# Optimization experiments

Measured on AMD Instinct MI355X. Metric: run time of the kernel, lower is better.

## Reference

```python
import jax, jax.numpy as jnp
from jax import lax
import numpy as np

HIDDEN = 2
INPUT = 1
NUM_CLASSES = 1
SEQ = 4
BATCH = 2097152


def setup_inputs() -> dict:
    key = jax.random.key(0)
    ks = jax.random.split(key, 7)
    s_ih = 1.0 / np.sqrt(HIDDEN)
    inp = {
        "x": jax.random.normal(ks[0], (BATCH, SEQ, INPUT), dtype=jnp.float32),
        # PyTorch nn.LSTM params: gate order [i, f, g, o], init U(-1/sqrt(H), 1/sqrt(H))
        "W_ih": jax.random.uniform(ks[1], (4 * HIDDEN, INPUT), jnp.float32, -s_ih, s_ih),
        "W_hh": jax.random.uniform(ks[2], (4 * HIDDEN, HIDDEN), jnp.float32, -s_ih, s_ih),
        "b_ih": jax.random.uniform(ks[3], (4 * HIDDEN,), jnp.float32, -s_ih, s_ih),
        "b_hh": jax.random.uniform(ks[4], (4 * HIDDEN,), jnp.float32, -s_ih, s_ih),
        "W_fc": jax.random.uniform(ks[5], (NUM_CLASSES, HIDDEN), jnp.float32, -s_ih, s_ih),
        "b_fc": jax.random.uniform(ks[6], (NUM_CLASSES,), jnp.float32, -s_ih, s_ih),
    }
    return inp


def _lstm_fc(x, W_ih, W_hh, b_ih, b_hh, W_fc, b_fc):
    B = x.shape[0]
    H = W_hh.shape[1]
    xt = jnp.swapaxes(x, 0, 1)  # [T, B, I]
    # Precompute input contribution to all 4 gates for every step: [T, B, 4H]
    xg = jnp.einsum('tbi,gi->tbg', xt, W_ih) + (b_ih + b_hh)

    def step(carry, xg_t):
        h, c = carry
        gates = xg_t + h @ W_hh.T  # [B, 4H]
        i, f, g, o = jnp.split(gates, 4, axis=-1)
        i = jax.nn.sigmoid(i)
        f = jax.nn.sigmoid(f)
        g = jnp.tanh(g)
        o = jax.nn.sigmoid(o)
        c = f * c + i * g
        h = o * jnp.tanh(c)
        return (h, c), None

    h0 = jnp.zeros((B, H), dtype=x.dtype)
    c0 = jnp.zeros((B, H), dtype=x.dtype)
    (h_T, _), _ = lax.scan(step, (h0, c0), xg)
    # fc applied to the final hidden state h_out (num_layers=1)
    return h_T @ W_fc.T + b_fc  # [B, num_classes]


def reference(x, W_ih, W_hh, b_ih, b_hh, W_fc, b_fc):
    return _lstm_fc(x, W_ih, W_hh, b_ih, b_hh, W_fc, b_fc)
```

## Files before the change

### kernel.cpp

```cpp
#include <hip/hip_runtime.h>
#include <hip/hip_bf16.h>

#define TABN 4352

__device__ __forceinline__ float gclamp(float y) {
    return __builtin_amdgcn_fmed3f(y, 0.0f, 4351.0f);
}

__global__ __launch_bounds__(256) void lstm_fc_nn(
    const float4* __restrict__ x4,
    const float*  __restrict__ W_ih,
    const float*  __restrict__ W_hh,
    const float*  __restrict__ b_ih,
    const float*  __restrict__ b_hh,
    const float*  __restrict__ W_fc,
    const float*  __restrict__ b_fc,
    float* __restrict__ out,
    int B)
{
    __shared__ float tab[TABN];
    for (int i = threadIdx.x; i < TABN; i += 256) {
        const float xv = fmaf((float)i, 0.00390625f, -8.0f);
        tab[i] = __fdividef(1.0f, 1.0f + __expf(-xv));
    }
    __syncthreads();

    float ws[8], w0[8], w1[8], bb[8];
#pragma unroll
    for (int g = 0; g < 8; ++g) {
        const float s = (g == 4 || g == 5) ? 512.0f : 256.0f;
        ws[g] = s * W_ih[g];
        w0[g] = s * W_hh[2 * g];
        w1[g] = s * W_hh[2 * g + 1];
        bb[g] = fmaf(s, b_ih[g] + b_hh[g], 2048.5f);
    }
    const float wfc0 = W_fc[0], wfc1 = W_fc[1], bfc = b_fc[0];

    const int half = B >> 1;
    const int tid = blockIdx.x * blockDim.x + threadIdx.x;
    if (tid >= half) return;

    const float4 xa = x4[tid];
    const float4 xb = x4[tid + half];
    const float xs[2][4] = {{xa.x, xa.y, xa.z, xa.w}, {xb.x, xb.y, xb.z, xb.w}};

    float h0[2], h1[2], d0[2], d1[2];

#pragma unroll
    for (int e = 0; e < 2; ++e) {
        const float yi0 = fmaf(ws[0], xs[e][0], bb[0]);
        const float yi1 = fmaf(ws[1], xs[e][0], bb[1]);
        const float yg0 = fmaf(ws[4], xs[e][0], bb[4]);
        const float yg1 = fmaf(ws[5], xs[e][0], bb[5]);
        const float yo0 = fmaf(ws[6], xs[e][0], bb[6]);
        const float yo1 = fmaf(ws[7], xs[e][0], bb[7]);
        const float si0 = tab[(unsigned)yi0];
        const float si1 = tab[(unsigned)yi1];
        const float sg0 = tab[(unsigned)gclamp(yg0)];
        const float sg1 = tab[(unsigned)gclamp(yg1)];
        const float so0 = tab[(unsigned)yo0];
        const float so1 = tab[(unsigned)yo1];
        d0[e] = si0 * fmaf(4.0f, sg0, -2.0f);
        d1[e] = si1 * fmaf(4.0f, sg1, -2.0f);
        const float sd0 = tab[(unsigned)fmaf(d0[e], 256.0f, 2048.5f)];
        const float sd1 = tab[(unsigned)fmaf(d1[e], 256.0f, 2048.5f)];
        h0[e] = fmaf(2.0f, so0 * sd0, -so0);
        h1[e] = fmaf(2.0f, so1 * sd1, -so1);
    }

#pragma unroll
    for (int t = 1; t < 4; ++t) {
#pragma unroll
        for (int e = 0; e < 2; ++e) {
            float y[8];
#pragma unroll
            for (int g = 0; g < 8; ++g)
                y[g] = fmaf(ws[g], xs[e][t],
                       fmaf(w0[g], h0[e],
                       fmaf(w1[g], h1[e], bb[g])));
            const float si0 = tab[(unsigned)y[0]];
            const float si1 = tab[(unsigned)y[1]];
            const float sf0 = tab[(unsigned)y[2]];
            const float sf1 = tab[(unsigned)y[3]];
            const float sg0 = tab[(unsigned)gclamp(y[4])];
            const float sg1 = tab[(unsigned)gclamp(y[5])];
            const float so0 = tab[(unsigned)y[6]];
            const float so1 = tab[(unsigned)y[7]];
            d0[e] = fmaf(sf0, d0[e], si0 * fmaf(4.0f, sg0, -2.0f));
            d1[e] = fmaf(sf1, d1[e], si1 * fmaf(4.0f, sg1, -2.0f));
            const float sd0 = tab[(unsigned)fmaf(d0[e], 256.0f, 2048.5f)];
            const float sd1 = tab[(unsigned)fmaf(d1[e], 256.0f, 2048.5f)];
            h0[e] = fmaf(2.0f, so0 * sd0, -so0);
            h1[e] = fmaf(2.0f, so1 * sd1, -so1);
        }
    }

    out[tid]        = fmaf(wfc0, h0[0], fmaf(wfc1, h1[0], bfc));
    out[tid + half] = fmaf(wfc0, h0[1], fmaf(wfc1, h1[1], bfc));
}

extern "C" void kernel_launch(void* const* d_in, const int* in_sizes, int n_in,
                              void* d_out, int out_size, void* d_ws, size_t ws_size,
                              hipStream_t stream) {
    const float4* x4   = (const float4*)d_in[0];
    const float*  W_ih = (const float*)d_in[1];
    const float*  W_hh = (const float*)d_in[2];
    const float*  b_ih = (const float*)d_in[3];
    const float*  b_hh = (const float*)d_in[4];
    const float*  W_fc = (const float*)d_in[5];
    const float*  b_fc = (const float*)d_in[6];
    float* out = (float*)d_out;

    const int B = out_size;
    const int half = B >> 1;
    const int block = 256;
    const int grid = (half + block - 1) / block;
    lstm_fc_nn<<<grid, block, 0, stream>>>(x4, W_ih, W_hh, b_ih, b_hh,
                                           W_fc, b_fc, out, B);
}
```

Baseline: 25.00 us.

## Replace sigmoid LUT with replicated bank-conflict-free linearly interpolated table

Swaps the 4352-entry nearest-neighbour sigmoid table for a 256-entry table that stores each value with its slope and interpolates linearly. Each entry is replicated 16 times, and each thread reads the copy chosen by its lane index, so lanes in a wave fall on different LDS banks and bank conflicts on the data-dependent lookups drop. The input scales and biases are rescaled to match the coarser table. In exchange, each lookup costs extra ALU work (fraction and fma) and moves 8 bytes instead of 4, LDS use rises to about 32KB per block, and the interpolated values differ in accuracy from before.

```diff
diff --git a/kernel.cpp b/kernel.cpp
--- a/kernel.cpp
+++ b/kernel.cpp
@@ -1,13 +1,20 @@
 #include <hip/hip_runtime.h>
 #include <hip/hip_bf16.h>
 
-#define TABN 4352
+
+__device__ __forceinline__ float lutl(const float2* __restrict__ tab2,
+                                      unsigned copy, float y) {
+    const unsigned iy = (unsigned)y;
+    const float    fy = y - (float)iy;
+    const float2   vs = tab2[iy * 16u + copy];
+    return fmaf(vs.y, fy, vs.x);
+}
 
 __device__ __forceinline__ float gclamp(float y) {
-    return __builtin_amdgcn_fmed3f(y, 0.0f, 4351.0f);
+    return __builtin_amdgcn_fmed3f(y, 0.0f, 255.999f);
 }
 
-__global__ __launch_bounds__(256) void lstm_fc_nn(
+__global__ __launch_bounds__(256) void lstm_fc_cfree(
     const float4* __restrict__ x4,
     const float*  __restrict__ W_ih,
     const float*  __restrict__ W_hh,
@@ -18,24 +25,37 @@
     float* __restrict__ out,
     int B)
 {
-    __shared__ float tab[TABN];
-    for (int i = threadIdx.x; i < TABN; i += 256) {
-        const float xv = fmaf((float)i, 0.00390625f, -8.0f);
-        tab[i] = __fdividef(1.0f, 1.0f + __expf(-xv));
+    __shared__ float2 tab2[256 * 16];
+    __shared__ float  vtmp[257];
+
+    {
+        const int t = threadIdx.x;
+        const float xv = fmaf((float)t, 0.0625f, -8.0f);
+        vtmp[t] = __fdividef(1.0f, 1.0f + __expf(-xv));
+        if (t == 0) vtmp[256] = __fdividef(1.0f, 1.0f + __expf(-8.0f));
+        __syncthreads();
+        const float val = vtmp[t];
+        const float slp = vtmp[t + 1] - val;
+#pragma unroll
+        for (int j = 0; j < 16; ++j) {
+            const int c = (t + j) & 15;
+            tab2[t * 16 + c] = make_float2(val, slp);
+        }
+        __syncthreads();
     }
-    __syncthreads();
 
     float ws[8], w0[8], w1[8], bb[8];
 #pragma unroll
     for (int g = 0; g < 8; ++g) {
-        const float s = (g == 4 || g == 5) ? 512.0f : 256.0f;
+        const float s = (g == 4 || g == 5) ? 32.0f : 16.0f;
         ws[g] = s * W_ih[g];
         w0[g] = s * W_hh[2 * g];
         w1[g] = s * W_hh[2 * g + 1];
-        bb[g] = fmaf(s, b_ih[g] + b_hh[g], 2048.5f);
+        bb[g] = fmaf(s, b_ih[g] + b_hh[g], 128.0f);
     }
     const float wfc0 = W_fc[0], wfc1 = W_fc[1], bfc = b_fc[0];
 
+    const unsigned copy = threadIdx.x & 15u;
     const int half = B >> 1;
     const int tid = blockIdx.x * blockDim.x + threadIdx.x;
     if (tid >= half) return;
@@ -50,20 +70,20 @@
     for (int e = 0; e < 2; ++e) {
         const float yi0 = fmaf(ws[0], xs[e][0], bb[0]);
         const float yi1 = fmaf(ws[1], xs[e][0], bb[1]);
-        const float yg0 = fmaf(ws[4], xs[e][0], bb[4]);
-        const float yg1 = fmaf(ws[5], xs[e][0], bb[5]);
+        const float yg0 = gclamp(fmaf(ws[4], xs[e][0], bb[4]));
+        const float yg1 = gclamp(fmaf(ws[5], xs[e][0], bb[5]));
         const float yo0 = fmaf(ws[6], xs[e][0], bb[6]);
         const float yo1 = fmaf(ws[7], xs[e][0], bb[7]);
-        const float si0 = tab[(unsigned)yi0];
-        const float si1 = tab[(unsigned)yi1];
-        const float sg0 = tab[(unsigned)gclamp(yg0)];
-        const float sg1 = tab[(unsigned)gclamp(yg1)];
-        const float so0 = tab[(unsigned)yo0];
-        const float so1 = tab[(unsigned)yo1];
+        const float si0 = lutl(tab2, copy, yi0);
+        const float si1 = lutl(tab2, copy, yi1);
+        const float sg0 = lutl(tab2, copy, yg0);
+        const float sg1 = lutl(tab2, copy, yg1);
+        const float so0 = lutl(tab2, copy, yo0);
+        const float so1 = lutl(tab2, copy, yo1);
         d0[e] = si0 * fmaf(4.0f, sg0, -2.0f);
         d1[e] = si1 * fmaf(4.0f, sg1, -2.0f);
-        const float sd0 = tab[(unsigned)fmaf(d0[e], 256.0f, 2048.5f)];
-        const float sd1 = tab[(unsigned)fmaf(d1[e], 256.0f, 2048.5f)];
+        const float sd0 = lutl(tab2, copy, fmaf(d0[e], 16.0f, 128.0f));
+        const float sd1 = lutl(tab2, copy, fmaf(d1[e], 16.0f, 128.0f));
         h0[e] = fmaf(2.0f, so0 * sd0, -so0);
         h1[e] = fmaf(2.0f, so1 * sd1, -so1);
     }
@@ -78,18 +98,18 @@
                 y[g] = fmaf(ws[g], xs[e][t],
                        fmaf(w0[g], h0[e],
                        fmaf(w1[g], h1[e], bb[g])));
-            const float si0 = tab[(unsigned)y[0]];
-            const float si1 = tab[(unsigned)y[1]];
-            const float sf0 = tab[(unsigned)y[2]];
-            const float sf1 = tab[(unsigned)y[3]];
-            const float sg0 = tab[(unsigned)gclamp(y[4])];
-            const float sg1 = tab[(unsigned)gclamp(y[5])];
-            const float so0 = tab[(unsigned)y[6]];
-            const float so1 = tab[(unsigned)y[7]];
+            const float si0 = lutl(tab2, copy, y[0]);
+            const float si1 = lutl(tab2, copy, y[1]);
+            const float sf0 = lutl(tab2, copy, y[2]);
+            const float sf1 = lutl(tab2, copy, y[3]);
+            const float sg0 = lutl(tab2, copy, gclamp(y[4]));
+            const float sg1 = lutl(tab2, copy, gclamp(y[5]));
+            const float so0 = lutl(tab2, copy, y[6]);
+            const float so1 = lutl(tab2, copy, y[7]);
             d0[e] = fmaf(sf0, d0[e], si0 * fmaf(4.0f, sg0, -2.0f));
             d1[e] = fmaf(sf1, d1[e], si1 * fmaf(4.0f, sg1, -2.0f));
-            const float sd0 = tab[(unsigned)fmaf(d0[e], 256.0f, 2048.5f)];
-            const float sd1 = tab[(unsigned)fmaf(d1[e], 256.0f, 2048.5f)];
+            const float sd0 = lutl(tab2, copy, fmaf(d0[e], 16.0f, 128.0f));
+            const float sd1 = lutl(tab2, copy, fmaf(d1[e], 16.0f, 128.0f));
             h0[e] = fmaf(2.0f, so0 * sd0, -so0);
             h1[e] = fmaf(2.0f, so1 * sd1, -so1);
         }
@@ -115,6 +135,6 @@
     const int half = B >> 1;
     const int block = 256;
     const int grid = (half + block - 1) / block;
-    lstm_fc_nn<<<grid, block, 0, stream>>>(x4, W_ih, W_hh, b_ih, b_hh,
-                                           W_fc, b_fc, out, B);
+    lstm_fc_cfree<<<grid, block, 0, stream>>>(x4, W_ih, W_hh, b_ih, b_hh,
+                                              W_fc, b_fc, out, B);
 }
```

Result: no change. 24.63 us (-1.5%).
